# Kernel optimization log

Hardware: AMD Instinct MI355X
Metric: run time of the kernel (lower is better)

The kernel has to match this reference:

```python
import jax, jax.numpy as jnp
import numpy as np

EMBED_DIM = 1024
NUM_HEADS = 16
HEAD_DIM = EMBED_DIM // NUM_HEADS
MAX_SEQ_LEN = 2048
ROPE_BASE = 10000.0


def _rope_tables(head_dim, max_seq_len, base):
    # inv_freq: (head_dim/2,)
    inv_freq = 1.0 / base ** (jnp.arange(0, head_dim, 2, dtype=jnp.float32) / head_dim)
    positions = jnp.arange(max_seq_len, dtype=jnp.float32)
    angles = positions[:, None] * inv_freq[None, :]  # (S, head_dim/2)
    # Original repeat_interleaves then slices [0::2], which recovers per-pair angles.
    return jnp.cos(angles), jnp.sin(angles)


def _apply_rope(x, cos, sin):
    # x: (B, H, S, D); cos/sin: (S, D/2)
    x_even = x[..., 0::2]
    x_odd = x[..., 1::2]
    c = cos[None, None, :, :]
    s = sin[None, None, :, :]
    x_even_rot = x_even * c - x_odd * s
    x_odd_rot = x_even * s + x_odd * c
    # interleave back: stack pairs on last dim and flatten
    x_rot = jnp.stack([x_even_rot, x_odd_rot], axis=-1)
    return x_rot.reshape(x.shape)


def setup_inputs() -> dict:
    key = jax.random.key(0)
    k1, k2, k3, k4 = jax.random.split(key, 4)
    B, S, E = 2, 2048, EMBED_DIM
    x = jax.random.normal(k1, (B, S, E), dtype=jnp.float32)
    bound_in = np.sqrt(6.0 / (3 * E + E)).astype(np.float32)
    in_proj_weight = jax.random.uniform(k2, (3 * E, E), minval=-bound_in, maxval=bound_in, dtype=jnp.float32)
    in_proj_bias = jnp.zeros((3 * E,), dtype=jnp.float32)
    bound_out = np.sqrt(6.0 / (E + E)).astype(np.float32)
    out_proj_weight = jax.random.uniform(k3, (E, E), minval=-bound_out, maxval=bound_out, dtype=jnp.float32)
    out_proj_bias = jnp.zeros((E,), dtype=jnp.float32)
    return {
        "query": x,
        "key": x,
        "value": x,
        "in_proj_weight": in_proj_weight,
        "in_proj_bias": in_proj_bias,
        "out_proj_weight": out_proj_weight,
        "out_proj_bias": out_proj_bias,
    }


def reference(query, key, value, in_proj_weight, in_proj_bias, out_proj_weight, out_proj_bias):
    B, S, E = query.shape
    H, D = NUM_HEADS, HEAD_DIM
    cos, sin = _rope_tables(D, MAX_SEQ_LEN, ROPE_BASE)
    cos, sin = cos[:S], sin[:S]

    # fused QKV projection (note: original applies in_proj to `query` only — self-attention)
    qkv = query @ in_proj_weight.T + in_proj_bias  # (B, S, 3E)
    q, k, v = jnp.split(qkv, 3, axis=-1)
    q = q.reshape(B, S, H, D).transpose(0, 2, 1, 3)  # (B, H, S, D)
    k = k.reshape(B, S, H, D).transpose(0, 2, 1, 3)
    v = v.reshape(B, S, H, D).transpose(0, 2, 1, 3)

    q = _apply_rope(q, cos, sin)
    k = _apply_rope(k, cos, sin)

    scale = 1.0 / np.sqrt(D).astype(np.float32)
    scores = jnp.einsum("bhqd,bhkd->bhqk", q, k) * scale
    attn = jax.nn.softmax(scores, axis=-1)
    out = jnp.einsum("bhqk,bhkd->bhqd", attn, v)  # (B, H, S, D)
    out = out.transpose(0, 2, 1, 3).reshape(B, S, E)
    return out @ out_proj_weight.T + out_proj_bias
```

## Files before the change

kernel.cpp:

```cpp
#include <hip/hip_runtime.h>
#include <hip/hip_bf16.h>
#include <cstdint>
#include <cstddef>

typedef __bf16 bf16;
typedef bf16 bf16x2 __attribute__((ext_vector_type(2)));
typedef bf16 bf16x4 __attribute__((ext_vector_type(4)));
typedef bf16 bf16x8 __attribute__((ext_vector_type(8)));
typedef float f32x4 __attribute__((ext_vector_type(4)));
typedef float f32x16 __attribute__((ext_vector_type(16)));

#define SEQ 2048
#define EMB 1024
#define NH 16
#define HD 64
#define BSZ 2
#define MROWS (BSZ*SEQ)

__device__ __forceinline__ void gload_lds16(const void* g, void* lds) {
  __builtin_amdgcn_global_load_lds((__attribute__((address_space(1))) void*)g,
                                   (__attribute__((address_space(3))) void*)lds,
                                   16, 0, 0);
}

__global__ void cvt3_kernel(const float* __restrict__ s0, bf16* __restrict__ d0, int n0_4,
                            const float* __restrict__ s1, bf16* __restrict__ d1, int n1_4,
                            const float* __restrict__ s2, bf16* __restrict__ d2, int n2_4) {
  int j = blockIdx.x * blockDim.x + threadIdx.x;
  const float* s; bf16* d;
  if (j < n0_4) { s = s0; d = d0; }
  else {
    j -= n0_4;
    if (j < n1_4) { s = s1; d = d1; }
    else { j -= n1_4; if (j >= n2_4) return; s = s2; d = d2; }
  }
  const float4 v = reinterpret_cast<const float4*>(s)[j];
  bf16x4 o;
  o[0] = (bf16)v.x; o[1] = (bf16)v.y; o[2] = (bf16)v.z; o[3] = (bf16)v.w;
  reinterpret_cast<bf16x4*>(d)[j] = o;
}

__global__ void rope_tables_kernel(float* __restrict__ cosT, float* __restrict__ sinT) {
  int idx = blockIdx.x * blockDim.x + threadIdx.x;
  if (idx >= SEQ * 32) return;
  int s = idx >> 5, j = idx & 31;
  float ex = (2.0f * (float)j) / 64.0f;
  float inv = 1.0f / powf(10000.0f, ex);
  float ang = (float)s * inv;
  cosT[idx] = cosf(ang);
  sinT[idx] = sinf(ang);
}

template<int EPI, int BM>
__launch_bounds__(256)
__global__ void gemm_bt(const bf16* __restrict__ A, const bf16* __restrict__ B,
                        const float* __restrict__ bias,
                        float* __restrict__ Cf,
                        bf16* __restrict__ qb, bf16* __restrict__ kb, bf16* __restrict__ vt,
                        const float* __restrict__ cosT, const float* __restrict__ sinT,
                        int Ndim, int Kdim) {
  constexpr int MREP = BM / 32;
  __shared__ __align__(16) bf16 Alds[BM * 32];
  __shared__ __align__(16) bf16 Blds[128 * 32];
  const int tid = threadIdx.x;
  const int wave = tid >> 6, lane = tid & 63;
  const int wr = wave >> 1, wc = wave & 1;
  const int bm = blockIdx.x * BM, bn = blockIdx.y * 128;

  f32x4 acc[MREP][4] = {};

  const int srow = lane >> 2;
  const int scol = (lane & 3) * 8;
  char* aldsb = (char*)Alds;
  char* bldsb = (char*)Blds;

  for (int kt = 0; kt < Kdim; kt += 32) {
#pragma unroll
    for (int c = 0; c < BM / 64; c++)
      gload_lds16(A + (size_t)(bm + (wave + 4 * c) * 16 + srow) * Kdim + kt + scol,
                  aldsb + wave * 1024 + c * 4096);
    gload_lds16(B + (size_t)(bn + wave * 16 + srow) * Kdim + kt + scol, bldsb + wave * 1024);
    gload_lds16(B + (size_t)(bn + (wave + 4) * 16 + srow) * Kdim + kt + scol, bldsb + wave * 1024 + 4096);
    __syncthreads();
    bf16x8 af[MREP], bfr[4];
#pragma unroll
    for (int m = 0; m < MREP; m++)
      af[m] = *reinterpret_cast<const bf16x8*>(Alds + (wr * (BM / 2) + m * 16 + (lane & 15)) * 32 + (lane >> 4) * 8);
#pragma unroll
    for (int n = 0; n < 4; n++)
      bfr[n] = *reinterpret_cast<const bf16x8*>(Blds + (wc * 64 + n * 16 + (lane & 15)) * 32 + (lane >> 4) * 8);
#pragma unroll
    for (int m = 0; m < MREP; m++)
#pragma unroll
      for (int n = 0; n < 4; n++)
        acc[m][n] = __builtin_amdgcn_mfma_f32_16x16x32_bf16(af[m], bfr[n], acc[m][n], 0, 0, 0);
    __syncthreads();
  }

#pragma unroll
  for (int m = 0; m < MREP; m++) {
#pragma unroll
    for (int n = 0; n < 4; n++) {
#pragma unroll
      for (int r = 0; r < 4; r++) {
        const int row = bm + wr * (BM / 2) + m * 16 + (lane >> 4) * 4 + r;
        const int col = bn + wc * 64 + n * 16 + (lane & 15);
        const float v = acc[m][n][r] + bias[col];
        if (EPI == 0) {
          Cf[(size_t)row * Ndim + col] = v;
        } else {
          const int b = row >> 11, s = row & (SEQ - 1);
          const int which = col >> 10, rem = col & 1023;
          const int h = rem >> 6, d = rem & 63;
          if (which == 2) {
            vt[(((size_t)(b * NH + h) * HD) + d) * SEQ + s] = (bf16)v;
          } else {
            const float vp = __shfl_xor(v, 1, 64);
            const int jj = d >> 1;
            const float c = cosT[(s << 5) + jj], sn = sinT[(s << 5) + jj];
            float vr = (d & 1) ? (vp * sn + v * c) : (v * c - vp * sn);
            if (which == 0) {
              vr *= 0.125f;
              qb[(((size_t)(b * NH + h) * SEQ) + s) * HD + d] = (bf16)vr;
            } else {
              kb[(((size_t)(b * NH + h) * SEQ) + s) * HD + d] = (bf16)vr;
            }
          }
        }
      }
    }
  }
}

__device__ __forceinline__ unsigned pk2(float a, float b) {
  bf16x2 t; t[0] = (bf16)a; t[1] = (bf16)b;
  unsigned u; __builtin_memcpy(&u, &t, 4); return u;
}

#define KPITCH 144

#define STAGE_LOAD(KV0) do { \
  kr0 = *(const int4*)(Kb + (size_t)((KV0) + (gtid >> 3)) * HD + (gtid & 7) * 8); \
  kr1 = *(const int4*)(Kb + (size_t)((KV0) + 32 + (gtid >> 3)) * HD + (gtid & 7) * 8); \
  vr0 = *(const int4*)(Vb + (size_t)(gtid >> 3) * SEQ + (KV0) + (gtid & 7) * 8); \
  vr1 = *(const int4*)(Vb + (size_t)(32 + (gtid >> 3)) * SEQ + (KV0) + (gtid & 7) * 8); \
} while (0)

#define STAGE_WRITE(BUF) do { \
  *(int4*)(Klds[grp][BUF] + (gtid >> 3) * KPITCH + (gtid & 7) * 16) = kr0; \
  *(int4*)(Klds[grp][BUF] + ((gtid >> 3) + 32) * KPITCH + (gtid & 7) * 16) = kr1; \
  const int vo_ = ((gtid & 7) >> 1) * 32 + ((gtid & 7) & 1) * 8; \
  char* v0p_ = Vlds[grp][BUF] + (gtid >> 3) * KPITCH + vo_; \
  char* v1p_ = Vlds[grp][BUF] + ((gtid >> 3) + 32) * KPITCH + vo_; \
  *(int2*)(v0p_)      = make_int2(vr0.x, vr0.y); \
  *(int2*)(v0p_ + 16) = make_int2(vr0.z, vr0.w); \
  *(int2*)(v1p_)      = make_int2(vr1.x, vr1.y); \
  *(int2*)(v1p_ + 16) = make_int2(vr1.z, vr1.w); \
} while (0)

#define COMPUTE_TILE64(BUFI) do { \
  const char* kbp = Klds[grp][BUFI]; const char* vbp = Vlds[grp][BUFI]; \
  bf16x8 KF[2][4], VF[2][4]; \
  _Pragma("unroll") \
  for (int hh = 0; hh < 2; hh++) \
    _Pragma("unroll") \
    for (int dk = 0; dk < 4; dk++) \
      KF[hh][dk] = *reinterpret_cast<const bf16x8*>(kbp + (hh * 32 + ql) * KPITCH + dk * 32 + hi * 16); \
  _Pragma("unroll") \
  for (int hh = 0; hh < 2; hh++) \
    _Pragma("unroll") \
    for (int i = 0; i < 4; i++) \
      VF[hh][i] = *reinterpret_cast<const bf16x8*>(vbp + ((i >> 1) * 32 + ql) * KPITCH + hh * 64 + (i & 1) * 32 + hi * 16); \
  f32x16 s0 = {}, s1 = {}; \
  __builtin_amdgcn_s_setprio(1); \
  _Pragma("unroll") \
  for (int dk = 0; dk < 4; dk++) { \
    s0 = __builtin_amdgcn_mfma_f32_32x32x16_bf16(KF[0][dk], qf[dk], s0, 0, 0, 0); \
    s1 = __builtin_amdgcn_mfma_f32_32x32x16_bf16(KF[1][dk], qf[dk], s1, 0, 0, 0); \
  } \
  __builtin_amdgcn_s_setprio(0); \
  float p0[16], p1[16]; \
  _Pragma("unroll") \
  for (int r = 0; r < 16; r++) { p0[r] = __expf(s0[r] - 12.f); p1[r] = __expf(s1[r] - 12.f); } \
   \
  bf16x8 pf[2][2]; \
  { \
    unsigned w00[4] = { pk2(p0[0], p0[1]),  pk2(p0[2], p0[3]),   pk2(p0[4], p0[5]),   pk2(p0[6], p0[7]) }; \
    unsigned w01[4] = { pk2(p0[8], p0[9]),  pk2(p0[10], p0[11]), pk2(p0[12], p0[13]), pk2(p0[14], p0[15]) }; \
    unsigned w10[4] = { pk2(p1[0], p1[1]),  pk2(p1[2], p1[3]),   pk2(p1[4], p1[5]),   pk2(p1[6], p1[7]) }; \
    unsigned w11[4] = { pk2(p1[8], p1[9]),  pk2(p1[10], p1[11]), pk2(p1[12], p1[13]), pk2(p1[14], p1[15]) }; \
    __builtin_memcpy(&pf[0][0], w00, 16); \
    __builtin_memcpy(&pf[0][1], w01, 16); \
    __builtin_memcpy(&pf[1][0], w10, 16); \
    __builtin_memcpy(&pf[1][1], w11, 16); \
  } \
  __builtin_amdgcn_s_setprio(1); \
  _Pragma("unroll") \
  for (int hh = 0; hh < 2; hh++) { \
    oacc0 = __builtin_amdgcn_mfma_f32_32x32x16_bf16(VF[hh][0], pf[hh][0], oacc0, 0, 0, 0); \
    oacc0 = __builtin_amdgcn_mfma_f32_32x32x16_bf16(VF[hh][1], pf[hh][1], oacc0, 0, 0, 0); \
    oacc1 = __builtin_amdgcn_mfma_f32_32x32x16_bf16(VF[hh][2], pf[hh][0], oacc1, 0, 0, 0); \
    oacc1 = __builtin_amdgcn_mfma_f32_32x32x16_bf16(VF[hh][3], pf[hh][1], oacc1, 0, 0, 0); \
    lacc  = __builtin_amdgcn_mfma_f32_32x32x16_bf16(onesf,    pf[hh][0], lacc,  0, 0, 0); \
    lacc  = __builtin_amdgcn_mfma_f32_32x32x16_bf16(onesf,    pf[hh][1], lacc,  0, 0, 0); \
  } \
  __builtin_amdgcn_s_setprio(0); \
} while (0)

__launch_bounds__(512)
__global__ void attn_kernel(const bf16* __restrict__ qb, const bf16* __restrict__ kb,
                            const bf16* __restrict__ vt, bf16* __restrict__ ob) {
  const int bid = (blockIdx.x & 7) * 64 + (blockIdx.x >> 3);
  const int qblk = bid & 15;
  const int bh = bid >> 4;
  const int b = bh >> 4, h = bh & 15;
  const int tid = threadIdx.x;
  const int wave = tid >> 6;
  const int grp = wave >> 2;
  const int wsub = wave & 3;
  const int gtid = tid & 255;
  const int lane = tid & 63;
  const int q0 = qblk * 128 + wsub * 32;
  const int ql = lane & 31, hi = lane >> 5;

  __shared__ __align__(16) char Klds[2][2][64 * KPITCH];
  __shared__ __align__(16) char Vlds[2][2][64 * KPITCH];

  const bf16* Qb = qb + (size_t)bh * SEQ * HD;
  const bf16* Kb = kb + (size_t)bh * SEQ * HD + (size_t)grp * 1024 * HD;
  const bf16* Vb = vt + (size_t)bh * HD * SEQ + grp * 1024;

  bf16x8 qf[4];
#pragma unroll
  for (int dk = 0; dk < 4; dk++)
    qf[dk] = *reinterpret_cast<const bf16x8*>(Qb + (size_t)(q0 + ql) * HD + dk * 16 + hi * 8);

  bf16x8 onesf;
#pragma unroll
  for (int i = 0; i < 8; i++) onesf[i] = (bf16)1.0f;

  f32x16 oacc0 = {}, oacc1 = {};
  f32x16 lacc = {};

  int4 kr0, kr1, vr0, vr1;
  STAGE_LOAD(0);
  STAGE_WRITE(0);
  __syncthreads();

  for (int t = 0; t < 16; ++t) {
    const int cur = t & 1;
    if (t < 15) STAGE_LOAD((t + 1) * 64);
    COMPUTE_TILE64(cur);
    if (t < 15) STAGE_WRITE(cur ^ 1);
    __syncthreads();
  }

  const float lrun = lacc[0];

  float* cb = (float*)(&Klds[0][0][0]);
  float* myb = cb + (wsub * 64 + lane) * 34;
  if (grp == 1) {
#pragma unroll
    for (int r = 0; r < 16; r++) { myb[r] = oacc0[r]; myb[16 + r] = oacc1[r]; }
    myb[32] = lrun;
  }
  __syncthreads();
  if (grp == 0) {
    const float inv = 1.0f / (lrun + myb[32]);
    const size_t orow = ((size_t)b * SEQ + q0 + ql) * EMB + h * HD;
#pragma unroll
    for (int r = 0; r < 16; r++) {
      const int d = (r & 3) + 8 * (r >> 2) + 4 * hi;
      ob[orow + d]      = (bf16)((oacc0[r] + myb[r]) * inv);
      ob[orow + 32 + d] = (bf16)((oacc1[r] + myb[16 + r]) * inv);
    }
  }
}

extern "C" void kernel_launch(void* const* d_in, const int* in_sizes, int n_in,
                              void* d_out, int out_size, void* d_ws, size_t ws_size,
                              hipStream_t stream) {
  const float* x    = (const float*)d_in[0];
  const float* Win  = (const float*)d_in[3];
  const float* bin  = (const float*)d_in[4];
  const float* Wout = (const float*)d_in[5];
  const float* bout = (const float*)d_in[6];
  float* out = (float*)d_out;

  char* p = (char*)d_ws;
  bf16* xb  = (bf16*)p; p += (size_t)MROWS * EMB * 2;
  bf16* wb  = (bf16*)p; p += (size_t)3 * EMB * EMB * 2;
  bf16* wob = (bf16*)p; p += (size_t)EMB * EMB * 2;
  bf16* qb  = (bf16*)p; p += (size_t)MROWS * EMB * 2;
  bf16* kb  = (bf16*)p; p += (size_t)MROWS * EMB * 2;
  bf16* vt  = (bf16*)p; p += (size_t)MROWS * EMB * 2;
  bf16* ob  = (bf16*)p; p += (size_t)MROWS * EMB * 2;
  float* cosT = (float*)p; p += (size_t)SEQ * 32 * 4;
  float* sinT = (float*)p; p += (size_t)SEQ * 32 * 4;

  const int n0 = MROWS * EMB / 4, n1 = 3 * EMB * EMB / 4, n2 = EMB * EMB / 4;
  cvt3_kernel<<<(n0 + n1 + n2 + 255) / 256, 256, 0, stream>>>(x, xb, n0, Win, wb, n1, Wout, wob, n2);
  rope_tables_kernel<<<(SEQ * 32 + 255) / 256, 256, 0, stream>>>(cosT, sinT);

  gemm_bt<1, 128><<<dim3(MROWS / 128, 3 * EMB / 128), 256, 0, stream>>>(
      xb, wb, bin, nullptr, qb, kb, vt, cosT, sinT, 3 * EMB, EMB);
  attn_kernel<<<BSZ * NH * (SEQ / 128), 512, 0, stream>>>(qb, kb, vt, ob);
  gemm_bt<0, 64><<<dim3(MROWS / 64, EMB / 128), 256, 0, stream>>>(
      ob, wob, bout, out, nullptr, nullptr, nullptr, nullptr, nullptr, EMB, EMB);
}
```

Baseline: 139.8 us.

## Fuse rope-table build into convert kernel, widen GEMM K-step, sum softmax denominators in VALU

Merges the rope-table generation into the fp32-to-bf16 conversion kernel, removing one launch. The GEMM now loads two 32-wide K slices per barrier pair into doubled LDS buffers, halving the number of syncthreads per K loop. In attention, the row-sum of exponentials is accumulated with per-lane VALU adds plus a cross-half shuffle instead of extra MFMAs against a ones vector. This trims MFMA work but adds VALU work and registers, and doubles GEMM LDS use, which may lower occupancy.

```diff
diff --git a/kernel.cpp b/kernel.cpp
--- a/kernel.cpp
+++ b/kernel.cpp
@@ -23,32 +23,36 @@
                                    16, 0, 0);
 }
 
-__global__ void cvt3_kernel(const float* __restrict__ s0, bf16* __restrict__ d0, int n0_4,
+__global__ void prep_kernel(const float* __restrict__ s0, bf16* __restrict__ d0, int n0_4,
                             const float* __restrict__ s1, bf16* __restrict__ d1, int n1_4,
-                            const float* __restrict__ s2, bf16* __restrict__ d2, int n2_4) {
+                            const float* __restrict__ s2, bf16* __restrict__ d2, int n2_4,
+                            float* __restrict__ cosT, float* __restrict__ sinT) {
   int j = blockIdx.x * blockDim.x + threadIdx.x;
   const float* s; bf16* d;
   if (j < n0_4) { s = s0; d = d0; }
   else {
-    j -= n0_4;
-    if (j < n1_4) { s = s1; d = d1; }
-    else { j -= n1_4; if (j >= n2_4) return; s = s2; d = d2; }
+    int j1 = j - n0_4;
+    if (j1 < n1_4) { s = s1; d = d1; j = j1; }
+    else {
+      int j2 = j1 - n1_4;
+      if (j2 < n2_4) { s = s2; d = d2; j = j2; }
+      else {
+        int idx = j2 - n2_4;
+        if (idx >= SEQ * 32) return;
+        int ss = idx >> 5, jj = idx & 31;
+        float ex = (2.0f * (float)jj) / 64.0f;
+        float inv = 1.0f / powf(10000.0f, ex);
+        float ang = (float)ss * inv;
+        cosT[idx] = cosf(ang);
+        sinT[idx] = sinf(ang);
+        return;
+      }
+    }
   }
   const float4 v = reinterpret_cast<const float4*>(s)[j];
   bf16x4 o;
   o[0] = (bf16)v.x; o[1] = (bf16)v.y; o[2] = (bf16)v.z; o[3] = (bf16)v.w;
   reinterpret_cast<bf16x4*>(d)[j] = o;
-}
-
-__global__ void rope_tables_kernel(float* __restrict__ cosT, float* __restrict__ sinT) {
-  int idx = blockIdx.x * blockDim.x + threadIdx.x;
-  if (idx >= SEQ * 32) return;
-  int s = idx >> 5, j = idx & 31;
-  float ex = (2.0f * (float)j) / 64.0f;
-  float inv = 1.0f / powf(10000.0f, ex);
-  float ang = (float)s * inv;
-  cosT[idx] = cosf(ang);
-  sinT[idx] = sinf(ang);
 }
 
 template<int EPI, int BM>
@@ -60,8 +64,8 @@
                         const float* __restrict__ cosT, const float* __restrict__ sinT,
                         int Ndim, int Kdim) {
   constexpr int MREP = BM / 32;
-  __shared__ __align__(16) bf16 Alds[BM * 32];
-  __shared__ __align__(16) bf16 Blds[128 * 32];
+  __shared__ __align__(16) bf16 Alds[2][BM * 32];
+  __shared__ __align__(16) bf16 Blds[2][128 * 32];
   const int tid = threadIdx.x;
   const int wave = tid >> 6, lane = tid & 63;
   const int wr = wave >> 1, wc = wave & 1;
@@ -71,29 +75,36 @@
 
   const int srow = lane >> 2;
   const int scol = (lane & 3) * 8;
-  char* aldsb = (char*)Alds;
-  char* bldsb = (char*)Blds;
-
-  for (int kt = 0; kt < Kdim; kt += 32) {
-#pragma unroll
-    for (int c = 0; c < BM / 64; c++)
-      gload_lds16(A + (size_t)(bm + (wave + 4 * c) * 16 + srow) * Kdim + kt + scol,
-                  aldsb + wave * 1024 + c * 4096);
-    gload_lds16(B + (size_t)(bn + wave * 16 + srow) * Kdim + kt + scol, bldsb + wave * 1024);
-    gload_lds16(B + (size_t)(bn + (wave + 4) * 16 + srow) * Kdim + kt + scol, bldsb + wave * 1024 + 4096);
+
+  for (int kt = 0; kt < Kdim; kt += 64) {
+#pragma unroll
+    for (int hf = 0; hf < 2; hf++) {
+      char* aldsb = (char*)Alds[hf];
+      char* bldsb = (char*)Blds[hf];
+      const int kc = kt + hf * 32;
+#pragma unroll
+      for (int c = 0; c < BM / 64; c++)
+        gload_lds16(A + (size_t)(bm + (wave + 4 * c) * 16 + srow) * Kdim + kc + scol,
+                    aldsb + wave * 1024 + c * 4096);
+      gload_lds16(B + (size_t)(bn + wave * 16 + srow) * Kdim + kc + scol, bldsb + wave * 1024);
+      gload_lds16(B + (size_t)(bn + (wave + 4) * 16 + srow) * Kdim + kc + scol, bldsb + wave * 1024 + 4096);
+    }
     __syncthreads();
-    bf16x8 af[MREP], bfr[4];
-#pragma unroll
-    for (int m = 0; m < MREP; m++)
-      af[m] = *reinterpret_cast<const bf16x8*>(Alds + (wr * (BM / 2) + m * 16 + (lane & 15)) * 32 + (lane >> 4) * 8);
-#pragma unroll
-    for (int n = 0; n < 4; n++)
-      bfr[n] = *reinterpret_cast<const bf16x8*>(Blds + (wc * 64 + n * 16 + (lane & 15)) * 32 + (lane >> 4) * 8);
-#pragma unroll
-    for (int m = 0; m < MREP; m++)
+#pragma unroll
+    for (int hf = 0; hf < 2; hf++) {
+      bf16x8 af[MREP], bfr[4];
+#pragma unroll
+      for (int m = 0; m < MREP; m++)
+        af[m] = *reinterpret_cast<const bf16x8*>(Alds[hf] + (wr * (BM / 2) + m * 16 + (lane & 15)) * 32 + (lane >> 4) * 8);
 #pragma unroll
       for (int n = 0; n < 4; n++)
-        acc[m][n] = __builtin_amdgcn_mfma_f32_16x16x32_bf16(af[m], bfr[n], acc[m][n], 0, 0, 0);
+        bfr[n] = *reinterpret_cast<const bf16x8*>(Blds[hf] + (wc * 64 + n * 16 + (lane & 15)) * 32 + (lane >> 4) * 8);
+#pragma unroll
+      for (int m = 0; m < MREP; m++)
+#pragma unroll
+        for (int n = 0; n < 4; n++)
+          acc[m][n] = __builtin_amdgcn_mfma_f32_16x16x32_bf16(af[m], bfr[n], acc[m][n], 0, 0, 0);
+    }
     __syncthreads();
   }
 
@@ -182,6 +193,8 @@
   float p0[16], p1[16]; \
   _Pragma("unroll") \
   for (int r = 0; r < 16; r++) { p0[r] = __expf(s0[r] - 12.f); p1[r] = __expf(s1[r] - 12.f); } \
+  _Pragma("unroll") \
+  for (int r = 0; r < 16; r++) psum[r] += p0[r] + p1[r]; \
    \
   bf16x8 pf[2][2]; \
   { \
@@ -201,8 +214,6 @@
     oacc0 = __builtin_amdgcn_mfma_f32_32x32x16_bf16(VF[hh][1], pf[hh][1], oacc0, 0, 0, 0); \
     oacc1 = __builtin_amdgcn_mfma_f32_32x32x16_bf16(VF[hh][2], pf[hh][0], oacc1, 0, 0, 0); \
     oacc1 = __builtin_amdgcn_mfma_f32_32x32x16_bf16(VF[hh][3], pf[hh][1], oacc1, 0, 0, 0); \
-    lacc  = __builtin_amdgcn_mfma_f32_32x32x16_bf16(onesf,    pf[hh][0], lacc,  0, 0, 0); \
-    lacc  = __builtin_amdgcn_mfma_f32_32x32x16_bf16(onesf,    pf[hh][1], lacc,  0, 0, 0); \
   } \
   __builtin_amdgcn_s_setprio(0); \
 } while (0)
@@ -235,12 +246,10 @@
   for (int dk = 0; dk < 4; dk++)
     qf[dk] = *reinterpret_cast<const bf16x8*>(Qb + (size_t)(q0 + ql) * HD + dk * 16 + hi * 8);
 
-  bf16x8 onesf;
-#pragma unroll
-  for (int i = 0; i < 8; i++) onesf[i] = (bf16)1.0f;
-
   f32x16 oacc0 = {}, oacc1 = {};
-  f32x16 lacc = {};
+  float psum[16];
+#pragma unroll
+  for (int r = 0; r < 16; r++) psum[r] = 0.f;
 
   int4 kr0, kr1, vr0, vr1;
   STAGE_LOAD(0);
@@ -255,7 +264,12 @@
     __syncthreads();
   }
 
-  const float lrun = lacc[0];
+#pragma unroll
+  for (int r = 0; r < 8; r++) psum[r] += psum[r + 8];
+#pragma unroll
+  for (int r = 0; r < 4; r++) psum[r] += psum[r + 4];
+  float lrun = (psum[0] + psum[1]) + (psum[2] + psum[3]);
+  lrun += __shfl_xor(lrun, 32, 64);
 
   float* cb = (float*)(&Klds[0][0][0]);
   float* myb = cb + (wsub * 64 + lane) * 34;
@@ -299,8 +313,8 @@
   float* sinT = (float*)p; p += (size_t)SEQ * 32 * 4;
 
   const int n0 = MROWS * EMB / 4, n1 = 3 * EMB * EMB / 4, n2 = EMB * EMB / 4;
-  cvt3_kernel<<<(n0 + n1 + n2 + 255) / 256, 256, 0, stream>>>(x, xb, n0, Win, wb, n1, Wout, wob, n2);
-  rope_tables_kernel<<<(SEQ * 32 + 255) / 256, 256, 0, stream>>>(cosT, sinT);
+  const int ntot = n0 + n1 + n2 + SEQ * 32;
+  prep_kernel<<<(ntot + 255) / 256, 256, 0, stream>>>(x, xb, n0, Win, wb, n1, Wout, wob, n2, cosT, sinT);
 
   gemm_bt<1, 128><<<dim3(MROWS / 128, 3 * EMB / 128), 256, 0, stream>>>(
       xb, wb, bin, nullptr, qb, kb, vt, cosT, sinT, 3 * EMB, EMB);
```

New measurement: 133.2 us. -4.7%, faster.
